# Kernel tuning notes

Hardware: AMD Instinct MI355X
Metric: run time of the kernel (lower is better)

## Reference

```python
import jax, jax.numpy as jnp
import numpy as np

B, S, H = 1, 2048, 1024
NH, HD = 16, 64
WIN = 512
M_MEM, M_PER = 512, 64
SCALE = 1.0 / np.sqrt(HD)
NEG_INF = jnp.float32(-1e30)


def setup_inputs() -> dict:
    key = jax.random.key(0)
    ks = jax.random.split(key, 22)
    std = 1.0 / np.sqrt(H)
    def w(k):
        return (jax.random.normal(k, (H, H), jnp.float32) * std)
    names = ['local_wq','local_wk','local_wv','local_wo',
             'long_wq','long_wk','long_wv','long_wo',
             'mem_wq','mem_wk','mem_wv','mem_wo',
             'per_wq','per_wk','per_wv','per_wo']
    d = {n: w(ks[i]) for i, n in enumerate(names)}
    d['gate_w'] = jax.random.normal(ks[16], (4 * H, 4), jnp.float32) * 0.02
    d['gate_b'] = jnp.zeros((4,), jnp.float32)
    d['x'] = jax.random.normal(ks[17], (B, S, H), jnp.float32)
    d['memory_kv'] = jax.random.normal(ks[18], (B, M_MEM, H), jnp.float32)
    d['persona_kv'] = jax.random.normal(ks[19], (B, M_PER, H), jnp.float32)
    return d


def _split_heads(t):
    # (B, T, H) -> (B, NH, T, HD)
    b, t_, _ = t.shape
    return t.reshape(b, t_, NH, HD).transpose(0, 2, 1, 3)


def _merge_heads(t):
    b, h, t_, d = t.shape
    return t.transpose(0, 2, 1, 3).reshape(b, t_, h * d)


def _self_attn(x, wq, wk, wv, wo, mask):
    # mask: (S, S) bool, True = masked out
    q = _split_heads(x @ wq)
    k = _split_heads(x @ wk)
    v = _split_heads(x @ wv)
    scores = jnp.einsum('bhsd,bhtd->bhst', q, k) * SCALE
    scores = jnp.where(mask[None, None], NEG_INF, scores)
    a = jax.nn.softmax(scores, axis=-1)
    out = jnp.einsum('bhst,bhtd->bhsd', a, v)
    return _merge_heads(out) @ wo


def _cross_attn(x, ctx, wq, wk, wv, wo):
    q = _split_heads(x @ wq)
    k = _split_heads(ctx @ wk)
    v = _split_heads(ctx @ wv)
    scores = jnp.einsum('bhsd,bhmd->bhsm', q, k) * SCALE
    a = jax.nn.softmax(scores, axis=-1)
    out = jnp.einsum('bhsm,bhmd->bhsd', a, v)
    return _merge_heads(out) @ wo


def reference(x, memory_kv, persona_kv,
              local_wq, local_wk, local_wv, local_wo,
              long_wq, long_wk, long_wv, long_wo,
              mem_wq, mem_wk, mem_wv, mem_wo,
              per_wq, per_wk, per_wv, per_wo,
              gate_w, gate_b):
    s = x.shape[1]
    idx = jnp.arange(s)
    causal = idx[None, :] > idx[:, None]                    # future tokens masked
    local = causal | ((idx[:, None] - idx[None, :]) > WIN)  # sliding window + causal

    local_out = _self_attn(x, local_wq, local_wk, local_wv, local_wo, local)
    long_out = _self_attn(x, long_wq, long_wk, long_wv, long_wo, causal)
    mem_out = _cross_attn(x, memory_kv, mem_wq, mem_wk, mem_wv, mem_wo)
    per_out = _cross_attn(x, persona_kv, per_wq, per_wk, per_wv, per_wo)

    outs = (local_out, long_out, mem_out, per_out)
    gate_in = jnp.concatenate(outs, axis=-1)                # (B, S, 4H)
    gates = jax.nn.softmax(gate_in @ gate_w + gate_b, axis=-1)  # (B, S, 4)
    fused = sum(gates[..., i:i + 1] * o for i, o in enumerate(outs))
    return fused  # emotion_scale = 1.0, dropout off (eval)
```

## Files before the change

### kernel.cpp

```cpp
#include <hip/hip_runtime.h>

#define S 2048
#define H 1024
#define NH 16
#define HD 64
#define WIN 512
#define SCALE_Q 0.18033688f
#define SM_SHIFT 16.0f

typedef unsigned short u16;
typedef unsigned int u32;
typedef __attribute__((ext_vector_type(8))) short bfrag;
typedef __attribute__((ext_vector_type(4))) float facc;
typedef __attribute__((ext_vector_type(4))) unsigned short u16x4;

constexpr size_t M1    = 1u << 20;
constexpr size_t WTO   = 0;
constexpr size_t XBO   = 8 * M1;
constexpr size_t MEMBO = 10 * M1;
constexpr size_t PERBO = MEMBO + (M1 >> 1);
constexpr size_t QO    = PERBO + (M1 >> 4);
constexpr size_t KVO   = QO + 8 * M1;
constexpr size_t K2O   = KVO + 8 * M1;
constexpr size_t V2O   = K2O + (M1 >> 1);
constexpr size_t K3O   = V2O + (M1 >> 1);
constexpr size_t V3O   = K3O + (M1 >> 4);
constexpr size_t VT1O  = V3O + (M1 >> 4);
constexpr size_t VT2O  = VT1O + 2 * M1;
constexpr size_t VT3O  = VT2O + (M1 >> 1);
constexpr size_t RECSZ = 8704;

__device__ __forceinline__ u16 f2bf(float f) {
    union { float f; unsigned u; } v; v.f = f;
    unsigned r = v.u + 0x7fffu + ((v.u >> 16) & 1u);
    return (u16)(r >> 16);
}
__device__ __forceinline__ float bf2f(u16 b) {
    union { unsigned u; float f; } v; v.u = ((unsigned)b) << 16;
    return v.f;
}
__device__ __forceinline__ void gload16(const u16* g, u16* l) {
    __builtin_amdgcn_global_load_lds(
        (const __attribute__((address_space(1))) u32*)g,
        (__attribute__((address_space(3))) u32*)l, 16, 0, 0);
}
__device__ __forceinline__ u32 cvt_pk(float a, float b) {
    u32 w;
    asm("v_cvt_pk_bf16_f32 %0, %1, %2" : "=v"(w) : "v"(a), "v"(b));
    return w;
}
__device__ __forceinline__ void blockbar() {
    __builtin_amdgcn_sched_barrier(0);
    asm volatile("" ::: "memory");
    __builtin_amdgcn_s_barrier();
    asm volatile("" ::: "memory");
    __builtin_amdgcn_sched_barrier(0);
}

__global__ __launch_bounds__(256)
void cast_all(const float* __restrict__ x, const float* __restrict__ mem,
              const float* __restrict__ per, u16* __restrict__ ws) {
    int i = blockIdx.x * 256 + threadIdx.x;
    const float* src; u16* dst;
    if (i < 262144)           { src = x;   dst = ws + XBO;   }
    else if (i < 327680)      { src = mem; dst = ws + MEMBO; i -= 262144; }
    else if (i < 335872)      { src = per; dst = ws + PERBO; i -= 327680; }
    else return;
    const float4* p = reinterpret_cast<const float4*>(src) + (size_t)i * 2;
    float4 a = p[0], b = p[1];
    u16x4 o0, o1;
    o0[0] = f2bf(a.x); o0[1] = f2bf(a.y); o0[2] = f2bf(a.z); o0[3] = f2bf(a.w);
    o1[0] = f2bf(b.x); o1[1] = f2bf(b.y); o1[2] = f2bf(b.z); o1[3] = f2bf(b.w);
    u16x4* q = reinterpret_cast<u16x4*>(dst) + (size_t)i * 2;
    q[0] = o0; q[1] = o1;
}

__global__ __launch_bounds__(256)
void transp_cast(const float* __restrict__ w0, const float* __restrict__ w1,
                 const float* __restrict__ w2, const float* __restrict__ w3,
                 u16* __restrict__ wt) {
    __shared__ float t[64][65];
    const float* w = blockIdx.z == 0 ? w0 : blockIdx.z == 1 ? w1
                   : blockIdx.z == 2 ? w2 : w3;
    u16* o = wt + (size_t)blockIdx.z * (1024 * 1024);
    const int kt = blockIdx.y * 64, nt = blockIdx.x * 64;
    const int r = threadIdx.x >> 4, c4 = (threadIdx.x & 15) * 4;
#pragma unroll
    for (int p = 0; p < 4; p++) {
        float4 v = *reinterpret_cast<const float4*>(
            &w[(size_t)(kt + r + p * 16) * 1024 + nt + c4]);
        t[r + p * 16][c4 + 0] = v.x; t[r + p * 16][c4 + 1] = v.y;
        t[r + p * 16][c4 + 2] = v.z; t[r + p * 16][c4 + 3] = v.w;
    }
    __syncthreads();
#pragma unroll
    for (int p = 0; p < 4; p++) {
        int nn = r + p * 16;
        u16x4 ov;
        ov[0] = f2bf(t[c4 + 0][nn]); ov[1] = f2bf(t[c4 + 1][nn]);
        ov[2] = f2bf(t[c4 + 2][nn]); ov[3] = f2bf(t[c4 + 3][nn]);
        *reinterpret_cast<u16x4*>(&o[(size_t)(nt + nn) * 1024 + kt + c4]) = ov;
    }
}

__global__ __launch_bounds__(256)
void transp_v(u16* __restrict__ ws) {
    const int z = blockIdx.z;
    const int Skv = (z < 2) ? 2048 : (z == 2 ? 512 : 64);
    const int kb = blockIdx.x;
    if (kb * 64 >= Skv) return;
    const int h = blockIdx.y;
    const u16* V = ws + (z == 0 ? KVO + 2 * M1 : z == 1 ? KVO + 6 * M1
                       : z == 2 ? V2O : V3O);
    u16* VT = ws + (z == 0 ? XBO : z == 1 ? VT1O : z == 2 ? VT2O : VT3O);
    __shared__ __align__(16) u16 t[64][72];
    {
        const int r = threadIdx.x >> 3, c8 = (threadIdx.x & 7) * 8;
#pragma unroll
        for (int p = 0; p < 2; p++) {
            int rr = r + p * 32;
            bfrag v = *reinterpret_cast<const bfrag*>(
                &V[(size_t)(kb * 64 + rr) * 1024 + h * 64 + c8]);
            *reinterpret_cast<bfrag*>(&t[rr][c8]) = v;
        }
    }
    __syncthreads();
    {
        const int d = threadIdx.x & 63;
        const int k8b = (threadIdx.x >> 6) * 8;
#pragma unroll
        for (int p = 0; p < 2; p++) {
            int k8 = k8b + p * 32;
            bfrag o;
#pragma unroll
            for (int j = 0; j < 8; j++) o[j] = (short)t[k8 + j][d];
            *reinterpret_cast<bfrag*>(
                &VT[(size_t)(h * 64 + d) * Skv + kb * 64 + k8]) = o;
        }
    }
}

__global__ __launch_bounds__(512, 2)
void gemm256(const u16* __restrict__ A, const u16* __restrict__ Bt,
             u16* __restrict__ C, long sB, long sC, int scaleMask) {
    __shared__ __align__(16) u16 sa[2][256 * 64];
    __shared__ __align__(16) u16 sb[2][256 * 64];
    Bt += (size_t)blockIdx.z * sB;
    C  += (size_t)blockIdx.z * sC;
    const float scl = ((scaleMask >> blockIdx.z) & 1) ? SCALE_Q : 1.0f;
    const int tid = threadIdx.x;
    const int wid = tid >> 6, lane = tid & 63;
    const int lhi = lane >> 4, llo = lane & 15;
    const int wm = wid >> 2, wn = wid & 3;
    const int row0 = blockIdx.y * 256, col0 = blockIdx.x * 256;

    facc acc[8][4];
#pragma unroll
    for (int i = 0; i < 8; i++)
#pragma unroll
        for (int j = 0; j < 4; j++)
#pragma unroll
            for (int k = 0; k < 4; k++) acc[i][j][k] = 0.f;

    auto stage = [&](int s, int kt) {
        const int k0 = kt * 64;
#pragma unroll
        for (int j = 0; j < 4; j++) {
            int i = j * 512 + tid;
            int r = i >> 3;
            int ck = (i & 7) ^ (r & 7);
            u16* da = &sa[s][(size_t)(j * 512 + wid * 64) * 8];
            u16* db = &sb[s][(size_t)(j * 512 + wid * 64) * 8];
            gload16(&A[(size_t)(row0 + r) * 1024 + k0 + ck * 8], da);
            gload16(&Bt[(size_t)(col0 + r) * 1024 + k0 + ck * 8], db);
        }
    };

    stage(0, 0);
    stage(1, 1);
    __builtin_amdgcn_sched_barrier(0);
    asm volatile("s_waitcnt vmcnt(8)" ::: "memory");
    blockbar();

    for (int j = 0; j < 16; j++) {
        const int sl = j & 1;
        const u16* pa = &sa[sl][0];
        const u16* pb = &sb[sl][0];
        bfrag bfr[2][4];
#pragma unroll
        for (int ks = 0; ks < 2; ks++) {
#pragma unroll
            for (int mg = 0; mg < 2; mg++) {
                bfrag af[4];
#pragma unroll
                for (int mf = 0; mf < 4; mf++) {
                    int r = wm * 128 + mg * 64 + mf * 16 + llo;
                    int p = (ks * 4 + lhi) ^ (r & 7);
                    af[mf] = *reinterpret_cast<const bfrag*>(&pa[r * 64 + p * 8]);
                }
                if (mg == 0) {
#pragma unroll
                    for (int nf = 0; nf < 4; nf++) {
                        int r = wn * 64 + nf * 16 + llo;
                        int p = (ks * 4 + lhi) ^ (r & 7);
                        bfr[ks][nf] = *reinterpret_cast<const bfrag*>(&pb[r * 64 + p * 8]);
                    }
                }
                __builtin_amdgcn_s_setprio(1);
#pragma unroll
                for (int mf = 0; mf < 4; mf++)
#pragma unroll
                    for (int nf = 0; nf < 4; nf++)
                        acc[mg * 4 + mf][nf] = __builtin_amdgcn_mfma_f32_16x16x32_bf16(
                            af[mf], bfr[ks][nf], acc[mg * 4 + mf][nf], 0, 0, 0);
                __builtin_amdgcn_s_setprio(0);
                blockbar();
            }
        }
        if (j + 2 < 16) {
            stage(sl, j + 2);
            __builtin_amdgcn_sched_barrier(0);
            asm volatile("s_waitcnt vmcnt(8)" ::: "memory");
            blockbar();
        } else if (j == 14) {
            asm volatile("s_waitcnt vmcnt(0)" ::: "memory");
            blockbar();
        }
    }

#pragma unroll
    for (int mf8 = 0; mf8 < 8; mf8++) {
#pragma unroll
        for (int r = 0; r < 4; r++) {
            int row = row0 + wm * 128 + mf8 * 16 + lhi * 4 + r;
#pragma unroll
            for (int nf = 0; nf < 4; nf++) {
                int col = col0 + wn * 64 + nf * 16 + llo;
                C[(size_t)row * 1024 + col] = f2bf(acc[mf8][nf][r] * scl);
            }
        }
    }
}

__global__ __launch_bounds__(256)
void gemm_bf16(const u16* __restrict__ A, const u16* __restrict__ Bt,
               u16* __restrict__ C, int M, long sA, long sB, long sC,
               int scaleMask) {
    __shared__ __align__(16) u16 sa[128 * 64];
    __shared__ __align__(16) u16 sb[128 * 64];
    A  += (size_t)blockIdx.z * sA;
    Bt += (size_t)blockIdx.z * sB;
    C  += (size_t)blockIdx.z * sC;
    const float scl = ((scaleMask >> blockIdx.z) & 1) ? SCALE_Q : 1.0f;
    const int tid = threadIdx.x;
    const int wid = tid >> 6, lane = tid & 63;
    const int lhi = lane >> 4, llo = lane & 15;
    const int wm = wid >> 1, wn = wid & 1;
    const int row0 = blockIdx.y * 128, col0 = blockIdx.x * 128;

    facc acc[4][4];
#pragma unroll
    for (int i = 0; i < 4; i++)
#pragma unroll
        for (int j = 0; j < 4; j++)
#pragma unroll
            for (int k = 0; k < 4; k++) acc[i][j][k] = 0.f;

    const int srow = lane >> 3, schunk = lane & 7;
    for (int kt = 0; kt < 16; kt++) {
        __syncthreads();
        const int k0 = kt * 64;
#pragma unroll
        for (int j = 0; j < 4; j++) {
            int r = wid * 32 + j * 8 + srow;
            int ck = schunk ^ (r & 7);
            int ar = row0 + r; if (ar > M - 1) ar = M - 1;
            gload16(&A[(size_t)ar * 1024 + k0 + ck * 8], &sa[(wid * 4 + j) * 512]);
            gload16(&Bt[(size_t)(col0 + r) * 1024 + k0 + ck * 8], &sb[(wid * 4 + j) * 512]);
        }
        __syncthreads();
#pragma unroll
        for (int ks = 0; ks < 2; ks++) {
            bfrag af[4], bfv[4];
#pragma unroll
            for (int mf = 0; mf < 4; mf++) {
                int r = wm * 64 + mf * 16 + llo;
                int p = (ks * 4 + lhi) ^ (r & 7);
                af[mf] = *reinterpret_cast<const bfrag*>(&sa[r * 64 + p * 8]);
            }
#pragma unroll
            for (int nf = 0; nf < 4; nf++) {
                int r = wn * 64 + nf * 16 + llo;
                int p = (ks * 4 + lhi) ^ (r & 7);
                bfv[nf] = *reinterpret_cast<const bfrag*>(&sb[r * 64 + p * 8]);
            }
            __builtin_amdgcn_s_setprio(1);
#pragma unroll
            for (int mf = 0; mf < 4; mf++)
#pragma unroll
                for (int nf = 0; nf < 4; nf++)
                    acc[mf][nf] = __builtin_amdgcn_mfma_f32_16x16x32_bf16(
                        af[mf], bfv[nf], acc[mf][nf], 0, 0, 0);
            __builtin_amdgcn_s_setprio(0);
        }
    }
#pragma unroll
    for (int mf = 0; mf < 4; mf++) {
#pragma unroll
        for (int r = 0; r < 4; r++) {
            int row = row0 + wm * 64 + mf * 16 + lhi * 4 + r;
            if (row < M) {
#pragma unroll
                for (int nf = 0; nf < 4; nf++) {
                    int col = col0 + wn * 64 + nf * 16 + llo;
                    C[(size_t)row * 1024 + col] = f2bf(acc[mf][nf][r] * scl);
                }
            }
        }
    }
}

__global__ __launch_bounds__(256)
void attn_tiled(u16* __restrict__ ws) {
    __shared__ __align__(16) u16 ksm[64 * 64];
    __shared__ __align__(16) u16 vtm[64 * 64];
    __shared__ __align__(16) u16 psm[4][16][72];

    const int blk = blockIdx.x;
    int branch, h, qb, pair = 0, half = 0;
    bool partial = false;
    if (blk < 256) {
        pair = blk >> 1; half = blk & 1;
        qb = 15 - (pair >> 4); h = pair & 15;
        branch = 1; partial = true;
    } else if (blk < 384) { int t = blk - 256; branch = 1; qb = 7 - (t >> 4);  h = t & 15; }
    else if (blk < 640)   { int t = blk - 384; branch = 0; qb = 15 - (t >> 4); h = t & 15; }
    else if (blk < 896)   { int t = blk - 640; branch = 2; qb = t >> 4;        h = t & 15; }
    else                  { int t = blk - 896; branch = 3; qb = t >> 4;        h = t & 15; }

    size_t kb_, vb_; int Skv, maskMode;
    if (branch == 0)      { kb_ = KVO;          vb_ = XBO;  Skv = 2048; maskMode = 2; }
    else if (branch == 1) { kb_ = KVO + 4 * M1; vb_ = VT1O; Skv = 2048; maskMode = 1; }
    else if (branch == 2) { kb_ = K2O;          vb_ = VT2O; Skv = 512;  maskMode = 0; }
    else                  { kb_ = K3O;          vb_ = VT3O; Skv = 64;   maskMode = 0; }
    const u16* Kp  = ws + kb_;
    const u16* VTp = ws + vb_;
    u16* Qp = ws + QO + (size_t)branch * 2 * M1;

    const int tid = threadIdx.x, wid = tid >> 6, lane = tid & 63;
    const int llo = lane & 15, lhi = lane >> 4;
    const int q0 = qb * 128;
    const int qw = q0 + wid * 32;
    const int hoff = h * 64;

    int tBeg, tEnd;
    if (partial) {
        int n = qb + 1;
        tBeg = half * n; tEnd = tBeg + n;
    } else {
        tEnd = maskMode ? (qb * 2 + 2) : (Skv >> 6);
        tBeg = (maskMode == 2 && q0 >= WIN) ? ((q0 - WIN) >> 6) : 0;
    }
    int myBeg = tBeg, myEnd = tEnd;
    if (maskMode) { int e = ((qw + 31) >> 6) + 1; if (e < myEnd) myEnd = e; }
    if (maskMode == 2 && qw >= WIN) { int b = (qw - WIN) >> 6; if (b > myBeg) myBeg = b; }

    bfrag qf[2][2];
#pragma unroll
    for (int sub = 0; sub < 2; sub++)
#pragma unroll
        for (int ds = 0; ds < 2; ds++)
            qf[sub][ds] = *reinterpret_cast<const bfrag*>(
                &Qp[(size_t)(qw + sub * 16 + llo) * 1024 + hoff + ds * 32 + lhi * 8]);

    facc ot[2][4];
    float lsum[2] = {0.f, 0.f};
#pragma unroll
    for (int sub = 0; sub < 2; sub++)
#pragma unroll
        for (int db = 0; db < 4; db++)
#pragma unroll
            for (int k = 0; k < 4; k++) ot[sub][db][k] = 0.f;

    const int srow = lane >> 3, schunk = lane & 7;

    for (int kt = tBeg; kt < tEnd; kt++) {
        __syncthreads();
#pragma unroll
        for (int j = 0; j < 2; j++) {
            int r = wid * 16 + j * 8 + srow;
            int ck = schunk ^ (r & 7);
            gload16(&Kp[(size_t)(kt * 64 + r) * 1024 + hoff + ck * 8],
                    &ksm[(wid * 2 + j) * 512]);
            gload16(&VTp[(size_t)(hoff + r) * Skv + kt * 64 + ck * 8],
                    &vtm[(wid * 2 + j) * 512]);
        }
        __syncthreads();

        if (kt >= myBeg && kt < myEnd) {
            bfrag kf[4][2], vf[4][2];
#pragma unroll
            for (int nf = 0; nf < 4; nf++)
#pragma unroll
                for (int ds = 0; ds < 2; ds++) {
                    int r = nf * 16 + llo;
                    int p = (ds * 4 + lhi) ^ (r & 7);
                    kf[nf][ds] = *reinterpret_cast<const bfrag*>(
                        &ksm[r * 64 + p * 8]);
                }
#pragma unroll
            for (int db = 0; db < 4; db++)
#pragma unroll
                for (int ks = 0; ks < 2; ks++) {
                    int d = db * 16 + llo;
                    int p = (ks * 4 + lhi) ^ (d & 7);
                    vf[db][ks] = *reinterpret_cast<const bfrag*>(
                        &vtm[d * 64 + p * 8]);
                }

#pragma unroll
            for (int sub = 0; sub < 2; sub++) {
                const int qsb = qw + sub * 16;
                facc st[4];
#pragma unroll
                for (int nf = 0; nf < 4; nf++)
#pragma unroll
                    for (int k = 0; k < 4; k++) st[nf][k] = 0.f;
                __builtin_amdgcn_s_setprio(1);
#pragma unroll
                for (int nf = 0; nf < 4; nf++)
#pragma unroll
                    for (int ds = 0; ds < 2; ds++)
                        st[nf] = __builtin_amdgcn_mfma_f32_16x16x32_bf16(
                            kf[nf][ds], qf[sub][ds], st[nf], 0, 0, 0);
                __builtin_amdgcn_s_setprio(0);

                float s[16];
#pragma unroll
                for (int nf = 0; nf < 4; nf++)
#pragma unroll
                    for (int r = 0; r < 4; r++) s[nf * 4 + r] = st[nf][r];

                const bool needC = maskMode && (kt * 64 + 63 > qsb);
                const bool needW = (maskMode == 2) && (kt * 64 < qsb + 15 - WIN);
                if (needC || needW) {
                    const int qi = qsb + llo;
#pragma unroll
                    for (int nf = 0; nf < 4; nf++)
#pragma unroll
                        for (int r = 0; r < 4; r++) {
                            int key = kt * 64 + nf * 16 + lhi * 4 + r;
                            if ((needC && key > qi) || (needW && (qi - key) > WIN))
                                s[nf * 4 + r] = -1e30f;
                        }
                }
                float p[16];
#pragma unroll
                for (int i = 0; i < 16; i++)
                    p[i] = __builtin_amdgcn_exp2f(s[i] - SM_SHIFT);
#pragma unroll
                for (int i = 0; i < 16; i++) lsum[sub] += p[i];

#pragma unroll
                for (int nf = 0; nf < 4; nf++)
#pragma unroll
                    for (int rp = 0; rp < 2; rp++) {
                        u32 w = cvt_pk(p[nf * 4 + rp * 2], p[nf * 4 + rp * 2 + 1]);
                        *reinterpret_cast<u32*>(
                            &psm[wid][llo][nf * 16 + lhi * 4 + rp * 2]) = w;
                    }
                bfrag pf0 = *reinterpret_cast<const bfrag*>(&psm[wid][llo][lhi * 8]);
                bfrag pf1 = *reinterpret_cast<const bfrag*>(&psm[wid][llo][32 + lhi * 8]);
                __builtin_amdgcn_s_setprio(1);
#pragma unroll
                for (int db = 0; db < 4; db++) {
                    ot[sub][db] = __builtin_amdgcn_mfma_f32_16x16x32_bf16(
                        vf[db][0], pf0, ot[sub][db], 0, 0, 0);
                    ot[sub][db] = __builtin_amdgcn_mfma_f32_16x16x32_bf16(
                        vf[db][1], pf1, ot[sub][db], 0, 0, 0);
                }
                __builtin_amdgcn_s_setprio(0);
            }
        }
    }

    if (!partial) {
#pragma unroll
        for (int sub = 0; sub < 2; sub++) {
            float l = lsum[sub];
            l += __shfl_xor(l, 16);
            l += __shfl_xor(l, 32);
            float inv = 1.f / l;
            u16* orow = &Qp[(size_t)(qw + sub * 16 + llo) * 1024 + hoff];
#pragma unroll
            for (int db = 0; db < 4; db++) {
                u16x4 pk;
#pragma unroll
                for (int r = 0; r < 4; r++) pk[r] = f2bf(ot[sub][db][r] * inv);
                *reinterpret_cast<u16x4*>(&orow[db * 16 + lhi * 4]) = pk;
            }
        }
    } else {
        float* rec = reinterpret_cast<float*>(ws) + (size_t)(pair * 2 + half) * RECSZ;
#pragma unroll
        for (int sub = 0; sub < 2; sub++) {
            float l = lsum[sub];
            l += __shfl_xor(l, 16);
            l += __shfl_xor(l, 32);
            rec[8192 + sub * 256 + tid] = l;
#pragma unroll
            for (int db = 0; db < 4; db++)
                *reinterpret_cast<facc*>(&rec[tid * 32 + sub * 16 + db * 4]) =
                    ot[sub][db];
        }
    }
}

__global__ __launch_bounds__(256)
void combine_split(u16* __restrict__ ws) {
    const int pair = blockIdx.x;
    const int qb = 15 - (pair >> 4), h = pair & 15;
    const int tid = threadIdx.x, wid = tid >> 6, lane = tid & 63;
    const int llo = lane & 15, lhi = lane >> 4;
    const float* r0 = reinterpret_cast<const float*>(ws) + (size_t)(pair * 2) * RECSZ;
    const float* r1 = r0 + RECSZ;
    u16* Qp = ws + QO + 2 * M1;
    const int qw = qb * 128 + wid * 32;
#pragma unroll
    for (int sub = 0; sub < 2; sub++) {
        float inv = 1.f / (r0[8192 + sub * 256 + tid] + r1[8192 + sub * 256 + tid]);
        u16* orow = &Qp[(size_t)(qw + sub * 16 + llo) * 1024 + h * 64];
#pragma unroll
        for (int db = 0; db < 4; db++) {
            u16x4 pk;
#pragma unroll
            for (int r = 0; r < 4; r++) {
                float v = r0[tid * 32 + sub * 16 + db * 4 + r] +
                          r1[tid * 32 + sub * 16 + db * 4 + r];
                pk[r] = f2bf(v * inv);
            }
            *reinterpret_cast<u16x4*>(&orow[db * 16 + lhi * 4]) = pk;
        }
    }
}

__global__ __launch_bounds__(256)
void gate_fuse(const u16* __restrict__ o4, const float* __restrict__ gw,
               const float* __restrict__ gb, float* __restrict__ out) {
    const int s = blockIdx.x, tid = threadIdx.x;
    const u16* ob0 = o4 + (size_t)s * H;
    float p[4] = {0.f, 0.f, 0.f, 0.f};
    for (int b = 0; b < 4; b++) {
        const u16* obb = ob0 + b * 2 * M1;
        const float* gwb = gw + (size_t)b * H * 4;
        for (int i = tid; i < H; i += 256) {
            float xv = bf2f(obb[i]);
            float4 g4 = *reinterpret_cast<const float4*>(&gwb[(size_t)i * 4]);
            p[0] += xv * g4.x; p[1] += xv * g4.y;
            p[2] += xv * g4.z; p[3] += xv * g4.w;
        }
    }
#pragma unroll
    for (int off = 1; off < 64; off <<= 1)
#pragma unroll
        for (int j = 0; j < 4; j++) p[j] += __shfl_xor(p[j], off);
    __shared__ float red[4][4];
    if ((tid & 63) == 0) {
        int w = tid >> 6;
#pragma unroll
        for (int j = 0; j < 4; j++) red[w][j] = p[j];
    }
    __syncthreads();
    float gl[4];
#pragma unroll
    for (int j = 0; j < 4; j++)
        gl[j] = gb[j] + red[0][j] + red[1][j] + red[2][j] + red[3][j];
    float mx = fmaxf(fmaxf(gl[0], gl[1]), fmaxf(gl[2], gl[3]));
    float e[4]; float tot = 0.f;
#pragma unroll
    for (int j = 0; j < 4; j++) { e[j] = __expf(gl[j] - mx); tot += e[j]; }
    float inv = 1.f / tot;
    int d = tid * 4;
    float4 rv; rv.x = rv.y = rv.z = rv.w = 0.f;
#pragma unroll
    for (int b = 0; b < 4; b++) {
        const u16* obb = ob0 + b * 2 * M1 + d;
        float wgt = e[b] * inv;
        rv.x += wgt * bf2f(obb[0]);
        rv.y += wgt * bf2f(obb[1]);
        rv.z += wgt * bf2f(obb[2]);
        rv.w += wgt * bf2f(obb[3]);
    }
    *reinterpret_cast<float4*>(&out[(size_t)s * H + d]) = rv;
}

extern "C" void kernel_launch(void* const* d_in, const int* in_sizes, int n_in,
                              void* d_out, int out_size, void* d_ws, size_t ws_size,
                              hipStream_t stream) {
    const float* Wm[16];
    for (int i = 0; i < 16; i++) Wm[i] = (const float*)d_in[i];
    const float* gw = (const float*)d_in[16];
    const float* gb = (const float*)d_in[17];
    const float* x = (const float*)d_in[18];
    const float* mem = (const float*)d_in[19];
    const float* per = (const float*)d_in[20];
    float* out = (float*)d_out;
    u16* ws = (u16*)d_ws;

    dim3 blk(256);
    cast_all<<<dim3(1312), blk, 0, stream>>>(x, mem, per, ws);

    transp_cast<<<dim3(16, 16, 4), blk, 0, stream>>>(
        Wm[0], Wm[4], Wm[8], Wm[12], ws + WTO);
    transp_cast<<<dim3(16, 16, 4), blk, 0, stream>>>(
        Wm[1], Wm[2], Wm[5], Wm[6], ws + WTO + 4 * M1);
    gemm256<<<dim3(4, 8, 8), dim3(512), 0, stream>>>(
        ws + XBO, ws + WTO, ws + QO, (long)M1, (long)(2 * M1), 0xF);

    transp_cast<<<dim3(16, 16, 4), blk, 0, stream>>>(
        Wm[9], Wm[10], Wm[13], Wm[14], ws + WTO);
    gemm_bf16<<<dim3(8, 4, 2), blk, 0, stream>>>(
        ws + MEMBO, ws + WTO, ws + K2O, 512, 0, (long)M1, (long)(M1 >> 1), 0);
    gemm_bf16<<<dim3(8, 1, 2), blk, 0, stream>>>(
        ws + PERBO, ws + WTO + 2 * M1, ws + K3O, 64, 0, (long)M1, (long)(M1 >> 4), 0);

    transp_v<<<dim3(32, 16, 4), blk, 0, stream>>>(ws);
    attn_tiled<<<dim3(1152), blk, 0, stream>>>(ws);
    combine_split<<<dim3(128), blk, 0, stream>>>(ws);

    transp_cast<<<dim3(16, 16, 4), blk, 0, stream>>>(
        Wm[3], Wm[7], Wm[11], Wm[15], ws + WTO);
    gemm_bf16<<<dim3(8, 16, 4), blk, 0, stream>>>(
        ws + QO, ws + WTO, ws + KVO, 2048, (long)(2 * M1), (long)M1,
        (long)(2 * M1), 0);

    gate_fuse<<<dim3(S), blk, 0, stream>>>(ws + KVO, gw, gb, out);
}
```

Measured before the change: 203.1 us.

## Deepen prefetch pipelines to four stages in GEMM and attention kernels

The 256x256 GEMM moves from a two-stage ring with K-tile 64 to a four-stage ring with K-tile 32. It prefetches three tiles ahead, splits the A and B loads around the MFMA groups, and uses a new swizzle for the 32-wide rows. The attention kernel goes from synchronous per-tile K/V loads bracketed by two __syncthreads to a four-buffer async ring with three tiles in flight and vmcnt-based waits. This aims to hide global-load latency behind MFMA work, but it raises LDS use (attention grows to 64KB of K/V buffers), which may lower occupancy.

```diff
diff --git a/kernel.cpp b/kernel.cpp
--- a/kernel.cpp
+++ b/kernel.cpp
@@ -13,6 +13,8 @@
 typedef __attribute__((ext_vector_type(8))) short bfrag;
 typedef __attribute__((ext_vector_type(4))) float facc;
 typedef __attribute__((ext_vector_type(4))) unsigned short u16x4;
+
+#define VMCNT(n) asm volatile("s_waitcnt vmcnt(" #n ")" ::: "memory")
 
 constexpr size_t M1    = 1u << 20;
 constexpr size_t WTO   = 0;
@@ -143,8 +145,8 @@
 __global__ __launch_bounds__(512, 2)
 void gemm256(const u16* __restrict__ A, const u16* __restrict__ Bt,
              u16* __restrict__ C, long sB, long sC, int scaleMask) {
-    __shared__ __align__(16) u16 sa[2][256 * 64];
-    __shared__ __align__(16) u16 sb[2][256 * 64];
+    __shared__ __align__(16) u16 sa[4][256 * 32];
+    __shared__ __align__(16) u16 sb[4][256 * 32];
     Bt += (size_t)blockIdx.z * sB;
     C  += (size_t)blockIdx.z * sC;
     const float scl = ((scaleMask >> blockIdx.z) & 1) ? SCALE_Q : 1.0f;
@@ -162,68 +164,84 @@
 #pragma unroll
             for (int k = 0; k < 4; k++) acc[i][j][k] = 0.f;
 
-    auto stage = [&](int s, int kt) {
-        const int k0 = kt * 64;
-#pragma unroll
-        for (int j = 0; j < 4; j++) {
-            int i = j * 512 + tid;
-            int r = i >> 3;
-            int ck = (i & 7) ^ (r & 7);
-            u16* da = &sa[s][(size_t)(j * 512 + wid * 64) * 8];
-            u16* db = &sb[s][(size_t)(j * 512 + wid * 64) * 8];
-            gload16(&A[(size_t)(row0 + r) * 1024 + k0 + ck * 8], da);
-            gload16(&Bt[(size_t)(col0 + r) * 1024 + k0 + ck * 8], db);
+    auto stageA = [&](int kt) {
+        const int s = kt & 3, k0 = kt * 32;
+#pragma unroll
+        for (int pass = 0; pass < 2; pass++) {
+            int i = pass * 512 + tid;
+            int r = i >> 2, c = i & 3;
+            int ck = c ^ ((r ^ (r >> 2)) & 3);
+            gload16(&A[(size_t)(row0 + r) * 1024 + k0 + ck * 8],
+                    &sa[s][(pass * 512 + wid * 64) * 8]);
         }
     };
-
-    stage(0, 0);
-    stage(1, 1);
+    auto stageB = [&](int kt) {
+        const int s = kt & 3, k0 = kt * 32;
+#pragma unroll
+        for (int pass = 0; pass < 2; pass++) {
+            int i = pass * 512 + tid;
+            int r = i >> 2, c = i & 3;
+            int ck = c ^ ((r ^ (r >> 2)) & 3);
+            gload16(&Bt[(size_t)(col0 + r) * 1024 + k0 + ck * 8],
+                    &sb[s][(pass * 512 + wid * 64) * 8]);
+        }
+    };
+
+    stageA(0); stageB(0);
+    stageA(1); stageB(1);
+    stageA(2); stageB(2);
     __builtin_amdgcn_sched_barrier(0);
-    asm volatile("s_waitcnt vmcnt(8)" ::: "memory");
+    VMCNT(8);
     blockbar();
 
-    for (int j = 0; j < 16; j++) {
-        const int sl = j & 1;
-        const u16* pa = &sa[sl][0];
-        const u16* pb = &sb[sl][0];
-        bfrag bfr[2][4];
-#pragma unroll
-        for (int ks = 0; ks < 2; ks++) {
-#pragma unroll
-            for (int mg = 0; mg < 2; mg++) {
-                bfrag af[4];
-#pragma unroll
-                for (int mf = 0; mf < 4; mf++) {
-                    int r = wm * 128 + mg * 64 + mf * 16 + llo;
-                    int p = (ks * 4 + lhi) ^ (r & 7);
-                    af[mf] = *reinterpret_cast<const bfrag*>(&pa[r * 64 + p * 8]);
-                }
-                if (mg == 0) {
-#pragma unroll
-                    for (int nf = 0; nf < 4; nf++) {
-                        int r = wn * 64 + nf * 16 + llo;
-                        int p = (ks * 4 + lhi) ^ (r & 7);
-                        bfr[ks][nf] = *reinterpret_cast<const bfrag*>(&pb[r * 64 + p * 8]);
-                    }
-                }
-                __builtin_amdgcn_s_setprio(1);
-#pragma unroll
-                for (int mf = 0; mf < 4; mf++)
-#pragma unroll
-                    for (int nf = 0; nf < 4; nf++)
-                        acc[mg * 4 + mf][nf] = __builtin_amdgcn_mfma_f32_16x16x32_bf16(
-                            af[mf], bfr[ks][nf], acc[mg * 4 + mf][nf], 0, 0, 0);
-                __builtin_amdgcn_s_setprio(0);
-                blockbar();
-            }
-        }
-        if (j + 2 < 16) {
-            stage(sl, j + 2);
+    for (int j = 0; j < 32; j++) {
+        const int s = j & 3;
+        const u16* pa = &sa[s][0];
+        const u16* pb = &sb[s][0];
+        const bool pre = (j + 3 < 32);
+        if (pre) stageA(j + 3);
+        bfrag bf[4];
+#pragma unroll
+        for (int nf = 0; nf < 4; nf++) {
+            int r = wn * 64 + nf * 16 + llo;
+            int p = lhi ^ ((r ^ (r >> 2)) & 3);
+            bf[nf] = *reinterpret_cast<const bfrag*>(&pb[r * 32 + p * 8]);
+        }
+        bfrag af[4];
+#pragma unroll
+        for (int mf = 0; mf < 4; mf++) {
+            int r = wm * 128 + mf * 16 + llo;
+            int p = lhi ^ ((r ^ (r >> 2)) & 3);
+            af[mf] = *reinterpret_cast<const bfrag*>(&pa[r * 32 + p * 8]);
+        }
+        __builtin_amdgcn_s_setprio(1);
+#pragma unroll
+        for (int mf = 0; mf < 4; mf++)
+#pragma unroll
+            for (int nf = 0; nf < 4; nf++)
+                acc[mf][nf] = __builtin_amdgcn_mfma_f32_16x16x32_bf16(
+                    af[mf], bf[nf], acc[mf][nf], 0, 0, 0);
+        __builtin_amdgcn_s_setprio(0);
+        if (pre) stageB(j + 3);
+#pragma unroll
+        for (int mf = 0; mf < 4; mf++) {
+            int r = wm * 128 + 64 + mf * 16 + llo;
+            int p = lhi ^ ((r ^ (r >> 2)) & 3);
+            af[mf] = *reinterpret_cast<const bfrag*>(&pa[r * 32 + p * 8]);
+        }
+        __builtin_amdgcn_s_setprio(1);
+#pragma unroll
+        for (int mf = 0; mf < 4; mf++)
+#pragma unroll
+            for (int nf = 0; nf < 4; nf++)
+                acc[4 + mf][nf] = __builtin_amdgcn_mfma_f32_16x16x32_bf16(
+                    af[mf], bf[nf], acc[4 + mf][nf], 0, 0, 0);
+        __builtin_amdgcn_s_setprio(0);
+        if (j < 31) {
             __builtin_amdgcn_sched_barrier(0);
-            asm volatile("s_waitcnt vmcnt(8)" ::: "memory");
-            blockbar();
-        } else if (j == 14) {
-            asm volatile("s_waitcnt vmcnt(0)" ::: "memory");
+            if (pre)              VMCNT(8);
+            else if (j == 29)     VMCNT(4);
+            else                  VMCNT(0);
             blockbar();
         }
     }
@@ -322,8 +340,8 @@
 
 __global__ __launch_bounds__(256)
 void attn_tiled(u16* __restrict__ ws) {
-    __shared__ __align__(16) u16 ksm[64 * 64];
-    __shared__ __align__(16) u16 vtm[64 * 64];
+    __shared__ __align__(16) u16 ksm[4][64 * 64];
+    __shared__ __align__(16) u16 vtm[4][64 * 64];
     __shared__ __align__(16) u16 psm[4][16][72];
 
     const int blk = blockIdx.x;
@@ -383,19 +401,32 @@
             for (int k = 0; k < 4; k++) ot[sub][db][k] = 0.f;
 
     const int srow = lane >> 3, schunk = lane & 7;
-
-    for (int kt = tBeg; kt < tEnd; kt++) {
-        __syncthreads();
+    auto stage = [&](int kt) {
+        const int s = kt & 3;
 #pragma unroll
         for (int j = 0; j < 2; j++) {
             int r = wid * 16 + j * 8 + srow;
             int ck = schunk ^ (r & 7);
             gload16(&Kp[(size_t)(kt * 64 + r) * 1024 + hoff + ck * 8],
-                    &ksm[(wid * 2 + j) * 512]);
+                    &ksm[s][(wid * 2 + j) * 512]);
             gload16(&VTp[(size_t)(hoff + r) * Skv + kt * 64 + ck * 8],
-                    &vtm[(wid * 2 + j) * 512]);
-        }
-        __syncthreads();
+                    &vtm[s][(wid * 2 + j) * 512]);
+        }
+    };
+
+    const int nt = tEnd - tBeg;
+    stage(tBeg);
+    if (nt > 1) stage(tBeg + 1);
+    if (nt > 2) stage(tBeg + 2);
+    __builtin_amdgcn_sched_barrier(0);
+    if (nt > 2)      VMCNT(8);
+    else if (nt > 1) VMCNT(4);
+    else             VMCNT(0);
+    blockbar();
+
+    for (int kt = tBeg; kt < tEnd; kt++) {
+        const int s = kt & 3;
+        if (kt + 3 < tEnd) stage(kt + 3);
 
         if (kt >= myBeg && kt < myEnd) {
             bfrag kf[4][2], vf[4][2];
@@ -406,7 +437,7 @@
                     int r = nf * 16 + llo;
                     int p = (ds * 4 + lhi) ^ (r & 7);
                     kf[nf][ds] = *reinterpret_cast<const bfrag*>(
-                        &ksm[r * 64 + p * 8]);
+                        &ksm[s][r * 64 + p * 8]);
                 }
 #pragma unroll
             for (int db = 0; db < 4; db++)
@@ -415,7 +446,7 @@
                     int d = db * 16 + llo;
                     int p = (ks * 4 + lhi) ^ (d & 7);
                     vf[db][ks] = *reinterpret_cast<const bfrag*>(
-                        &vtm[d * 64 + p * 8]);
+                        &vtm[s][d * 64 + p * 8]);
                 }
 
 #pragma unroll
@@ -435,11 +466,11 @@
                             kf[nf][ds], qf[sub][ds], st[nf], 0, 0, 0);
                 __builtin_amdgcn_s_setprio(0);
 
-                float s[16];
+                float sarr[16];
 #pragma unroll
                 for (int nf = 0; nf < 4; nf++)
 #pragma unroll
-                    for (int r = 0; r < 4; r++) s[nf * 4 + r] = st[nf][r];
+                    for (int r = 0; r < 4; r++) sarr[nf * 4 + r] = st[nf][r];
 
                 const bool needC = maskMode && (kt * 64 + 63 > qsb);
                 const bool needW = (maskMode == 2) && (kt * 64 < qsb + 15 - WIN);
@@ -451,13 +482,13 @@
                         for (int r = 0; r < 4; r++) {
                             int key = kt * 64 + nf * 16 + lhi * 4 + r;
                             if ((needC && key > qi) || (needW && (qi - key) > WIN))
-                                s[nf * 4 + r] = -1e30f;
+                                sarr[nf * 4 + r] = -1e30f;
                         }
                 }
                 float p[16];
 #pragma unroll
                 for (int i = 0; i < 16; i++)
-                    p[i] = __builtin_amdgcn_exp2f(s[i] - SM_SHIFT);
+                    p[i] = __builtin_amdgcn_exp2f(sarr[i] - SM_SHIFT);
 #pragma unroll
                 for (int i = 0; i < 16; i++) lsum[sub] += p[i];
 
@@ -481,6 +512,13 @@
                 }
                 __builtin_amdgcn_s_setprio(0);
             }
+        }
+        if (kt + 1 < tEnd) {
+            __builtin_amdgcn_sched_barrier(0);
+            if (kt + 3 < tEnd)      VMCNT(8);
+            else if (kt + 2 < tEnd) VMCNT(4);
+            else                    VMCNT(0);
+            blockbar();
         }
     }
 
```

New measurement: 208.3 us. 1.03x slower.

## Restructure gemm256 pipeline into quarter-step staged loads and merge small launches

Applied to the files above, without the earlier changes.

The 256x256 GEMM main loop is reorganised into four quarter steps per k-tile. Each quarter issues part of the next tile's global-to-LDS loads (B halves, then A row groups) and waits on finer vmcnt counts, so loads overlap MFMA work instead of being staged two tiles ahead in bulk. Separately, the two weight-transpose launches are merged into one 8-slice launch, and the memory and persona K/V projections are merged into a single gemm_small launch to cut launch overhead. The finer synchronisation adds more block barriers per tile and relies on the vmcnt accounting being exactly right.

```diff
diff --git a/kernel.cpp b/kernel.cpp
--- a/kernel.cpp
+++ b/kernel.cpp
@@ -13,6 +13,8 @@
 typedef __attribute__((ext_vector_type(8))) short bfrag;
 typedef __attribute__((ext_vector_type(4))) float facc;
 typedef __attribute__((ext_vector_type(4))) unsigned short u16x4;
+
+#define VMCNT(n) asm volatile("s_waitcnt vmcnt(" #n ")" ::: "memory")
 
 constexpr size_t M1    = 1u << 20;
 constexpr size_t WTO   = 0;
@@ -76,12 +78,14 @@
 }
 
 __global__ __launch_bounds__(256)
-void transp_cast(const float* __restrict__ w0, const float* __restrict__ w1,
-                 const float* __restrict__ w2, const float* __restrict__ w3,
-                 u16* __restrict__ wt) {
+void transp_cast8(const float* __restrict__ w0, const float* __restrict__ w1,
+                  const float* __restrict__ w2, const float* __restrict__ w3,
+                  const float* __restrict__ w4, const float* __restrict__ w5,
+                  const float* __restrict__ w6, const float* __restrict__ w7,
+                  u16* __restrict__ wt) {
     __shared__ float t[64][65];
-    const float* w = blockIdx.z == 0 ? w0 : blockIdx.z == 1 ? w1
-                   : blockIdx.z == 2 ? w2 : w3;
+    const float* wp[8] = {w0, w1, w2, w3, w4, w5, w6, w7};
+    const float* w = wp[blockIdx.z];
     u16* o = wt + (size_t)blockIdx.z * (1024 * 1024);
     const int kt = blockIdx.y * 64, nt = blockIdx.x * 64;
     const int r = threadIdx.x >> 4, c4 = (threadIdx.x & 15) * 4;
@@ -162,81 +166,170 @@
 #pragma unroll
             for (int k = 0; k < 4; k++) acc[i][j][k] = 0.f;
 
-    auto stage = [&](int s, int kt) {
-        const int k0 = kt * 64;
-#pragma unroll
-        for (int j = 0; j < 4; j++) {
-            int i = j * 512 + tid;
-            int r = i >> 3;
+    auto stageB = [&](int kt, int h) {
+        const int b = kt & 1, k0 = kt * 64;
+#pragma unroll
+        for (int pass = 0; pass < 2; pass++) {
+            int i = pass * 512 + tid;
+            int r = h * 128 + (i >> 3);
             int ck = (i & 7) ^ (r & 7);
-            u16* da = &sa[s][(size_t)(j * 512 + wid * 64) * 8];
-            u16* db = &sb[s][(size_t)(j * 512 + wid * 64) * 8];
-            gload16(&A[(size_t)(row0 + r) * 1024 + k0 + ck * 8], da);
-            gload16(&Bt[(size_t)(col0 + r) * 1024 + k0 + ck * 8], db);
+            gload16(&Bt[(size_t)(col0 + r) * 1024 + k0 + ck * 8],
+                    &sb[b][(size_t)(h * 1024 + pass * 512 + wid * 64) * 8]);
         }
     };
-
-    stage(0, 0);
-    stage(1, 1);
+    auto stageAg = [&](int kt, int g) {
+        const int b = kt & 1, k0 = kt * 64;
+#pragma unroll
+        for (int pass = 0; pass < 2; pass++) {
+            int i = pass * 512 + tid;
+            int i8 = i >> 3;
+            int r = g * 64 + (i8 & 63) + (i8 >> 6) * 128;
+            int ck = (i & 7) ^ (r & 7);
+            int b8 = (pass * 512 + wid * 64) >> 3;
+            int rb = g * 64 + (b8 & 63) + (b8 >> 6) * 128;
+            gload16(&A[(size_t)(row0 + r) * 1024 + k0 + ck * 8],
+                    &sa[b][(size_t)rb * 64]);
+        }
+    };
+
+    stageB(0, 0); stageB(0, 1); stageAg(0, 0); stageAg(0, 1);
     __builtin_amdgcn_sched_barrier(0);
-    asm volatile("s_waitcnt vmcnt(8)" ::: "memory");
+    VMCNT(2);
     blockbar();
 
     for (int j = 0; j < 16; j++) {
-        const int sl = j & 1;
-        const u16* pa = &sa[sl][0];
-        const u16* pb = &sb[sl][0];
-        bfrag bfr[2][4];
-#pragma unroll
-        for (int ks = 0; ks < 2; ks++) {
-#pragma unroll
-            for (int mg = 0; mg < 2; mg++) {
-                bfrag af[4];
-#pragma unroll
-                for (int mf = 0; mf < 4; mf++) {
-                    int r = wm * 128 + mg * 64 + mf * 16 + llo;
-                    int p = (ks * 4 + lhi) ^ (r & 7);
-                    af[mf] = *reinterpret_cast<const bfrag*>(&pa[r * 64 + p * 8]);
-                }
-                if (mg == 0) {
-#pragma unroll
-                    for (int nf = 0; nf < 4; nf++) {
+        const int b = j & 1;
+        const u16* pa = &sa[b][0];
+        const u16* pb = &sb[b][0];
+        bfrag bf[4][2];
+#pragma unroll
+        for (int q = 0; q < 4; q++) {
+            if (q == 0) {
+#pragma unroll
+                for (int nf = 0; nf < 4; nf++)
+#pragma unroll
+                    for (int ks = 0; ks < 2; ks++) {
                         int r = wn * 64 + nf * 16 + llo;
                         int p = (ks * 4 + lhi) ^ (r & 7);
-                        bfr[ks][nf] = *reinterpret_cast<const bfrag*>(&pb[r * 64 + p * 8]);
+                        bf[nf][ks] = *reinterpret_cast<const bfrag*>(
+                            &pb[r * 64 + p * 8]);
                     }
+            }
+            bfrag af[2][2];
+#pragma unroll
+            for (int rr = 0; rr < 2; rr++)
+#pragma unroll
+                for (int ks = 0; ks < 2; ks++) {
+                    int r = wm * 128 + (q * 2 + rr) * 16 + llo;
+                    int p = (ks * 4 + lhi) ^ (r & 7);
+                    af[rr][ks] = *reinterpret_cast<const bfrag*>(
+                        &pa[r * 64 + p * 8]);
                 }
-                __builtin_amdgcn_s_setprio(1);
-#pragma unroll
-                for (int mf = 0; mf < 4; mf++)
-#pragma unroll
-                    for (int nf = 0; nf < 4; nf++)
-                        acc[mg * 4 + mf][nf] = __builtin_amdgcn_mfma_f32_16x16x32_bf16(
-                            af[mf], bfr[ks][nf], acc[mg * 4 + mf][nf], 0, 0, 0);
-                __builtin_amdgcn_s_setprio(0);
-                blockbar();
-            }
-        }
-        if (j + 2 < 16) {
-            stage(sl, j + 2);
+            if (j < 15) {
+                if (q == 0)      stageB(j + 1, 0);
+                else if (q == 1) stageB(j + 1, 1);
+                else if (q == 2) stageAg(j + 1, 0);
+                else             stageAg(j + 1, 1);
+            }
+            blockbar();
+            asm volatile("s_waitcnt lgkmcnt(0)" ::: "memory");
             __builtin_amdgcn_sched_barrier(0);
-            asm volatile("s_waitcnt vmcnt(8)" ::: "memory");
+            __builtin_amdgcn_s_setprio(1);
+#pragma unroll
+            for (int rr = 0; rr < 2; rr++)
+#pragma unroll
+                for (int nf = 0; nf < 4; nf++)
+#pragma unroll
+                    for (int ks = 0; ks < 2; ks++)
+                        acc[q * 2 + rr][nf] = __builtin_amdgcn_mfma_f32_16x16x32_bf16(
+                            af[rr][ks], bf[nf][ks], acc[q * 2 + rr][nf], 0, 0, 0);
+            __builtin_amdgcn_s_setprio(0);
+            __builtin_amdgcn_sched_barrier(0);
+            if (q == 1) { if (j < 15) { VMCNT(4); } else { VMCNT(0); } }
+            else if (q == 3 && j < 15) { VMCNT(2); }
             blockbar();
-        } else if (j == 14) {
-            asm volatile("s_waitcnt vmcnt(0)" ::: "memory");
-            blockbar();
-        }
-    }
-
-#pragma unroll
-    for (int mf8 = 0; mf8 < 8; mf8++) {
+        }
+    }
+
+#pragma unroll
+    for (int mf = 0; mf < 8; mf++) {
 #pragma unroll
         for (int r = 0; r < 4; r++) {
-            int row = row0 + wm * 128 + mf8 * 16 + lhi * 4 + r;
+            int row = row0 + wm * 128 + mf * 16 + lhi * 4 + r;
 #pragma unroll
             for (int nf = 0; nf < 4; nf++) {
                 int col = col0 + wn * 64 + nf * 16 + llo;
-                C[(size_t)row * 1024 + col] = f2bf(acc[mf8][nf][r] * scl);
+                C[(size_t)row * 1024 + col] = f2bf(acc[mf][nf][r] * scl);
+            }
+        }
+    }
+}
+
+__device__ __forceinline__ void gemm128_body(
+    const u16* __restrict__ A, const u16* __restrict__ Bt, u16* __restrict__ C,
+    int M, float scl, u16* sa, u16* sb, int row0, int col0) {
+    const int tid = threadIdx.x;
+    const int wid = tid >> 6, lane = tid & 63;
+    const int lhi = lane >> 4, llo = lane & 15;
+    const int wm = wid >> 1, wn = wid & 1;
+
+    facc acc[4][4];
+#pragma unroll
+    for (int i = 0; i < 4; i++)
+#pragma unroll
+        for (int j = 0; j < 4; j++)
+#pragma unroll
+            for (int k = 0; k < 4; k++) acc[i][j][k] = 0.f;
+
+    const int srow = lane >> 3, schunk = lane & 7;
+    for (int kt = 0; kt < 16; kt++) {
+        __syncthreads();
+        const int k0 = kt * 64;
+#pragma unroll
+        for (int j = 0; j < 4; j++) {
+            int r = wid * 32 + j * 8 + srow;
+            int ck = schunk ^ (r & 7);
+            int ar = row0 + r; if (ar > M - 1) ar = M - 1;
+            gload16(&A[(size_t)ar * 1024 + k0 + ck * 8], &sa[(wid * 4 + j) * 512]);
+            gload16(&Bt[(size_t)(col0 + r) * 1024 + k0 + ck * 8], &sb[(wid * 4 + j) * 512]);
+        }
+        __syncthreads();
+#pragma unroll
+        for (int ks = 0; ks < 2; ks++) {
+            bfrag af[4], bfv[4];
+#pragma unroll
+            for (int mf = 0; mf < 4; mf++) {
+                int r = wm * 64 + mf * 16 + llo;
+                int p = (ks * 4 + lhi) ^ (r & 7);
+                af[mf] = *reinterpret_cast<const bfrag*>(&sa[r * 64 + p * 8]);
+            }
+#pragma unroll
+            for (int nf = 0; nf < 4; nf++) {
+                int r = wn * 64 + nf * 16 + llo;
+                int p = (ks * 4 + lhi) ^ (r & 7);
+                bfv[nf] = *reinterpret_cast<const bfrag*>(&sb[r * 64 + p * 8]);
+            }
+            __builtin_amdgcn_s_setprio(1);
+#pragma unroll
+            for (int mf = 0; mf < 4; mf++)
+#pragma unroll
+                for (int nf = 0; nf < 4; nf++)
+                    acc[mf][nf] = __builtin_amdgcn_mfma_f32_16x16x32_bf16(
+                        af[mf], bfv[nf], acc[mf][nf], 0, 0, 0);
+            __builtin_amdgcn_s_setprio(0);
+        }
+    }
+#pragma unroll
+    for (int mf = 0; mf < 4; mf++) {
+#pragma unroll
+        for (int r = 0; r < 4; r++) {
+            int row = row0 + wm * 64 + mf * 16 + lhi * 4 + r;
+            if (row < M) {
+#pragma unroll
+                for (int nf = 0; nf < 4; nf++) {
+                    int col = col0 + wn * 64 + nf * 16 + llo;
+                    C[(size_t)row * 1024 + col] = f2bf(acc[mf][nf][r] * scl);
+                }
             }
         }
     }
@@ -252,72 +345,20 @@
     Bt += (size_t)blockIdx.z * sB;
     C  += (size_t)blockIdx.z * sC;
     const float scl = ((scaleMask >> blockIdx.z) & 1) ? SCALE_Q : 1.0f;
-    const int tid = threadIdx.x;
-    const int wid = tid >> 6, lane = tid & 63;
-    const int lhi = lane >> 4, llo = lane & 15;
-    const int wm = wid >> 1, wn = wid & 1;
-    const int row0 = blockIdx.y * 128, col0 = blockIdx.x * 128;
-
-    facc acc[4][4];
-#pragma unroll
-    for (int i = 0; i < 4; i++)
-#pragma unroll
-        for (int j = 0; j < 4; j++)
-#pragma unroll
-            for (int k = 0; k < 4; k++) acc[i][j][k] = 0.f;
-
-    const int srow = lane >> 3, schunk = lane & 7;
-    for (int kt = 0; kt < 16; kt++) {
-        __syncthreads();
-        const int k0 = kt * 64;
-#pragma unroll
-        for (int j = 0; j < 4; j++) {
-            int r = wid * 32 + j * 8 + srow;
-            int ck = schunk ^ (r & 7);
-            int ar = row0 + r; if (ar > M - 1) ar = M - 1;
-            gload16(&A[(size_t)ar * 1024 + k0 + ck * 8], &sa[(wid * 4 + j) * 512]);
-            gload16(&Bt[(size_t)(col0 + r) * 1024 + k0 + ck * 8], &sb[(wid * 4 + j) * 512]);
-        }
-        __syncthreads();
-#pragma unroll
-        for (int ks = 0; ks < 2; ks++) {
-            bfrag af[4], bfv[4];
-#pragma unroll
-            for (int mf = 0; mf < 4; mf++) {
-                int r = wm * 64 + mf * 16 + llo;
-                int p = (ks * 4 + lhi) ^ (r & 7);
-                af[mf] = *reinterpret_cast<const bfrag*>(&sa[r * 64 + p * 8]);
-            }
-#pragma unroll
-            for (int nf = 0; nf < 4; nf++) {
-                int r = wn * 64 + nf * 16 + llo;
-                int p = (ks * 4 + lhi) ^ (r & 7);
-                bfv[nf] = *reinterpret_cast<const bfrag*>(&sb[r * 64 + p * 8]);
-            }
-            __builtin_amdgcn_s_setprio(1);
-#pragma unroll
-            for (int mf = 0; mf < 4; mf++)
-#pragma unroll
-                for (int nf = 0; nf < 4; nf++)
-                    acc[mf][nf] = __builtin_amdgcn_mfma_f32_16x16x32_bf16(
-                        af[mf], bfv[nf], acc[mf][nf], 0, 0, 0);
-            __builtin_amdgcn_s_setprio(0);
-        }
-    }
-#pragma unroll
-    for (int mf = 0; mf < 4; mf++) {
-#pragma unroll
-        for (int r = 0; r < 4; r++) {
-            int row = row0 + wm * 64 + mf * 16 + lhi * 4 + r;
-            if (row < M) {
-#pragma unroll
-                for (int nf = 0; nf < 4; nf++) {
-                    int col = col0 + wn * 64 + nf * 16 + llo;
-                    C[(size_t)row * 1024 + col] = f2bf(acc[mf][nf][r] * scl);
-                }
-            }
-        }
-    }
+    gemm128_body(A, Bt, C, M, scl, sa, sb, blockIdx.y * 128, blockIdx.x * 128);
+}
+
+__global__ __launch_bounds__(256)
+void gemm_small(u16* __restrict__ ws) {
+    const int z = blockIdx.z;
+    if (z >= 2 && blockIdx.y > 0) return;
+    __shared__ __align__(16) u16 sa[128 * 64];
+    __shared__ __align__(16) u16 sb[128 * 64];
+    const u16* A = ws + ((z < 2) ? MEMBO : PERBO);
+    const int M = (z < 2) ? 512 : 64;
+    const u16* Bt = ws + WTO + (size_t)z * M1;
+    u16* C = ws + (z == 0 ? K2O : z == 1 ? V2O : z == 2 ? K3O : V3O);
+    gemm128_body(A, Bt, C, M, 1.0f, sa, sb, blockIdx.y * 128, blockIdx.x * 128);
 }
 
 __global__ __launch_bounds__(256)
@@ -610,26 +651,21 @@
     dim3 blk(256);
     cast_all<<<dim3(1312), blk, 0, stream>>>(x, mem, per, ws);
 
-    transp_cast<<<dim3(16, 16, 4), blk, 0, stream>>>(
-        Wm[0], Wm[4], Wm[8], Wm[12], ws + WTO);
-    transp_cast<<<dim3(16, 16, 4), blk, 0, stream>>>(
-        Wm[1], Wm[2], Wm[5], Wm[6], ws + WTO + 4 * M1);
+    transp_cast8<<<dim3(16, 16, 8), blk, 0, stream>>>(
+        Wm[0], Wm[4], Wm[8], Wm[12], Wm[1], Wm[2], Wm[5], Wm[6], ws + WTO);
     gemm256<<<dim3(4, 8, 8), dim3(512), 0, stream>>>(
         ws + XBO, ws + WTO, ws + QO, (long)M1, (long)(2 * M1), 0xF);
 
-    transp_cast<<<dim3(16, 16, 4), blk, 0, stream>>>(
-        Wm[9], Wm[10], Wm[13], Wm[14], ws + WTO);
-    gemm_bf16<<<dim3(8, 4, 2), blk, 0, stream>>>(
-        ws + MEMBO, ws + WTO, ws + K2O, 512, 0, (long)M1, (long)(M1 >> 1), 0);
-    gemm_bf16<<<dim3(8, 1, 2), blk, 0, stream>>>(
-        ws + PERBO, ws + WTO + 2 * M1, ws + K3O, 64, 0, (long)M1, (long)(M1 >> 4), 0);
+    transp_cast8<<<dim3(16, 16, 4), blk, 0, stream>>>(
+        Wm[9], Wm[10], Wm[13], Wm[14], Wm[9], Wm[10], Wm[13], Wm[14], ws + WTO);
+    gemm_small<<<dim3(8, 4, 4), blk, 0, stream>>>(ws);
 
     transp_v<<<dim3(32, 16, 4), blk, 0, stream>>>(ws);
     attn_tiled<<<dim3(1152), blk, 0, stream>>>(ws);
     combine_split<<<dim3(128), blk, 0, stream>>>(ws);
 
-    transp_cast<<<dim3(16, 16, 4), blk, 0, stream>>>(
-        Wm[3], Wm[7], Wm[11], Wm[15], ws + WTO);
+    transp_cast8<<<dim3(16, 16, 4), blk, 0, stream>>>(
+        Wm[3], Wm[7], Wm[11], Wm[15], Wm[3], Wm[7], Wm[11], Wm[15], ws + WTO);
     gemm_bf16<<<dim3(8, 16, 4), blk, 0, stream>>>(
         ws + QO, ws + WTO, ws + KVO, 2048, (long)(2 * M1), (long)M1,
         (long)(2 * M1), 0);
```

After: 174.4 us, median of 2. 1.16x faster.
